# Kernel optimization log

Hardware: AMD Instinct MI355X
Metric: run time of the kernel (lower is better)

Reference implementation:

```python
import jax, jax.numpy as jnp
import numpy as np

EMBED_DIM = 1024
NUM_HEADS = 16
HEAD_DIM = EMBED_DIM // NUM_HEADS
B, L = 2, 2048
SCALE = HEAD_DIM ** -0.5


def setup_inputs() -> dict:
    key = jax.random.key(0)
    ks = jax.random.split(key, 8)
    x = jax.random.normal(ks[0], (B, L, EMBED_DIM), dtype=jnp.float32)
    phylo_dists = jax.random.uniform(ks[1], (B, L), dtype=jnp.float32)
    alibi_bias = jax.random.normal(ks[2], (NUM_HEADS, L, L), dtype=jnp.float32) * 0.02
    # causal mask: 1 where attending allowed (j <= i), broadcast over B,H
    attn_mask = (jnp.arange(L)[:, None] >= jnp.arange(L)[None, :])[None, None]
    # learned params (Linear stores weight as [out, in]; y = x @ W.T + b)
    qkv_w = jax.random.normal(ks[3], (3 * EMBED_DIM, EMBED_DIM), dtype=jnp.float32) * (EMBED_DIM ** -0.5)
    qkv_b = jnp.zeros((3 * EMBED_DIM,), dtype=jnp.float32)
    out_w = jax.random.normal(ks[4], (EMBED_DIM, EMBED_DIM), dtype=jnp.float32) * (EMBED_DIM ** -0.5)
    out_b = jnp.zeros((EMBED_DIM,), dtype=jnp.float32)
    phylo_alpha = jnp.float32(0.5)
    return {"x": x, "phylo_dists": phylo_dists, "alibi_bias": alibi_bias,
            "attn_mask": attn_mask, "qkv_w": qkv_w, "qkv_b": qkv_b,
            "out_w": out_w, "out_b": out_b, "phylo_alpha": phylo_alpha}


def reference(x, phylo_dists, alibi_bias, attn_mask, qkv_w, qkv_b, out_w, out_b, phylo_alpha):
    Bm, Lm, D = x.shape
    qkv = (x @ qkv_w.T + qkv_b).reshape(Bm, Lm, 3, NUM_HEADS, HEAD_DIM)
    qkv = jnp.transpose(qkv, (2, 0, 3, 1, 4))  # [3, B, H, L, hd]
    q, k, v = qkv[0], qkv[1], qkv[2]
    # phylo temperature: scalar per batch element
    phylo_scalar = phylo_dists.mean(axis=-1).reshape(Bm, 1, 1, 1)
    temp = jnp.clip(1.0 + phylo_alpha * phylo_scalar, 1e-6, None)
    scores = jnp.einsum('bhqd,bhkd->bhqk', q, k) * (SCALE * temp)
    scores = scores + alibi_bias[None]  # [B,H,L,L]
    scores = jnp.where(attn_mask, scores, -jnp.inf)
    attn = jax.nn.softmax(scores, axis=-1)
    out = jnp.einsum('bhqk,bhkd->bhqd', attn, v)
    out = jnp.transpose(out, (0, 2, 1, 3)).reshape(Bm, Lm, D)
    return out @ out_w.T + out_b
```

## Files before the change

### kernel.cpp

```cpp
#include <hip/hip_runtime.h>
#include <hip/hip_bf16.h>

typedef __attribute__((ext_vector_type(8))) short bf16x8;
typedef __attribute__((ext_vector_type(4))) float f32x4;
typedef __attribute__((ext_vector_type(4))) float f4v;
typedef __attribute__((ext_vector_type(4))) short s4v;

__device__ __forceinline__ short f2bf(float f) {
    union { __hip_bfloat16 h; short s; } u;
    u.h = __float2bfloat16(f);
    return u.s;
}

__device__ __forceinline__ void gload_lds16(const void* g, void* l) {
    __builtin_amdgcn_global_load_lds(
        (const __attribute__((address_space(1))) void*)g,
        (__attribute__((address_space(3))) void*)l,
        16, 0, 0);
}

#define MFMA16(a, b, c) __builtin_amdgcn_mfma_f32_16x16x32_bf16((a), (b), (c), 0, 0, 0)

__global__ void prep_kernel(const float* __restrict__ x,
                            const float* __restrict__ qw,
                            const float* __restrict__ ow,
                            const float* __restrict__ pd,
                            const float* __restrict__ alphap,
                            s4v* __restrict__ xb, s4v* __restrict__ qb,
                            s4v* __restrict__ ob, float* __restrict__ scales) {
    __shared__ float wsum[4];
    if (blockIdx.x >= 2048) {
        int b = blockIdx.x - 2048;
        float s = 0.f;
        for (int i = threadIdx.x; i < 2048; i += 256) s += pd[b * 2048 + i];
        for (int o = 32; o; o >>= 1) s += __shfl_down(s, o);
        if ((threadIdx.x & 63) == 0) wsum[threadIdx.x >> 6] = s;
        __syncthreads();
        if (threadIdx.x == 0) {
            float t = wsum[0] + wsum[1] + wsum[2] + wsum[3];
            float mean = t * (1.0f / 2048.0f);
            float temp = fmaxf(1.0f + alphap[0] * mean, 1e-6f);
            scales[b] = 0.125f * temp;
        }
        return;
    }
    #pragma unroll
    for (int j = 0; j < 4; ++j) {
        int idx = blockIdx.x * 1024 + j * 256 + threadIdx.x;
        const f4v* src;
        s4v* dst;
        int off;
        if (idx < 1048576)      { src = (const f4v*)x;  dst = xb; off = idx; }
        else if (idx < 1835008) { src = (const f4v*)qw; dst = qb; off = idx - 1048576; }
        else                    { src = (const f4v*)ow; dst = ob; off = idx - 1835008; }
        f4v v = src[off];
        s4v o;
        #pragma unroll
        for (int k = 0; k < 4; ++k) o[k] = f2bf(v[k]);
        dst[off] = o;
    }
}

template<int BF16_OUT, int NF>
__global__ __launch_bounds__(256, 2)
void gemm_nt(const __hip_bfloat16* __restrict__ A,
             const __hip_bfloat16* __restrict__ Bw,
             const float* __restrict__ bias,
             void* __restrict__ Cv,
             int M, int N, int K) {
    __shared__ short sA[128 * 64];
    __shared__ short sB[NF * 32 * 64];
    const int tid = threadIdx.x;
    const int wave = tid >> 6, lane = tid & 63;
    const int g = lane >> 4, c = lane & 15;
    const int wr = wave >> 1, wc = wave & 1;
    const long m0 = (long)blockIdx.y * 128, n0 = (long)blockIdx.x * (NF * 32);

    f32x4 acc[4][NF];
    #pragma unroll
    for (int m = 0; m < 4; ++m)
        #pragma unroll
        for (int n = 0; n < NF; ++n) acc[m][n] = f32x4{0.f, 0.f, 0.f, 0.f};

    for (int k0 = 0; k0 < K; k0 += 64) {
        #pragma unroll
        for (int i = 0; i < 4; ++i) {
            int cb = (i * 4 + wave) * 64;
            int chunk = cb + lane;
            int row = chunk >> 3;
            int sc = ((chunk & 7) * 16) ^ ((row & 7) << 4);
            const char* gA = (const char*)(A + (m0 + row) * (long)K + k0) + sc;
            gload_lds16(gA, (char*)sA + cb * 16);
        }
        #pragma unroll
        for (int i = 0; i < NF; ++i) {
            int cb = (i * 4 + wave) * 64;
            int chunk = cb + lane;
            int row = chunk >> 3;
            int sc = ((chunk & 7) * 16) ^ ((row & 7) << 4);
            const char* gB = (const char*)(Bw + (n0 + row) * (long)K + k0) + sc;
            gload_lds16(gB, (char*)sB + cb * 16);
        }
        __syncthreads();
        #pragma unroll
        for (int s = 0; s < 2; ++s) {
            bf16x8 af[4], bfr[NF];
            #pragma unroll
            for (int m = 0; m < 4; ++m) {
                int row = wr * 64 + m * 16 + c;
                int kb = (s * 64 + g * 16) ^ ((row & 7) << 4);
                af[m] = *(const bf16x8*)((const char*)sA + row * 128 + kb);
            }
            #pragma unroll
            for (int n = 0; n < NF; ++n) {
                int row = wc * (NF * 16) + n * 16 + c;
                int kb = (s * 64 + g * 16) ^ ((row & 7) << 4);
                bfr[n] = *(const bf16x8*)((const char*)sB + row * 128 + kb);
            }
            #pragma unroll
            for (int m = 0; m < 4; ++m)
                #pragma unroll
                for (int n = 0; n < NF; ++n)
                    acc[m][n] = MFMA16(af[m], bfr[n], acc[m][n]);
        }
        __syncthreads();
    }

    #pragma unroll
    for (int m = 0; m < 4; ++m) {
        #pragma unroll
        for (int n = 0; n < NF; ++n) {
            long col = n0 + wc * (NF * 16) + n * 16 + c;
            float bv = bias[col];
            #pragma unroll
            for (int r = 0; r < 4; ++r) {
                long row = m0 + wr * 64 + m * 16 + g * 4 + r;
                float v = acc[m][n][r] + bv;
                if (BF16_OUT)
                    ((__hip_bfloat16*)Cv)[row * N + col] = __float2bfloat16(v);
                else
                    ((float*)Cv)[row * N + col] = v;
            }
        }
    }
}


__device__ __forceinline__ void compute_tile(
    const bf16x8 (&kf)[4][2], const short* sVtc, short* sPw,
    bf16x8 qf0, bf16x8 qf1,
    f32x4 (&acc_o)[4], f32x4& accL, float (&m)[4],
    const float (&ab)[4][4],
    float scale, int qi0, int kv0, bool diag, int g, int c)
{
    f32x4 accs[4];
    #pragma unroll
    for (int nf = 0; nf < 4; ++nf) {
        accs[nf] = f32x4{0.f, 0.f, 0.f, 0.f};
        accs[nf] = MFMA16(qf0, kf[nf][0], accs[nf]);
        accs[nf] = MFMA16(qf1, kf[nf][1], accs[nf]);
    }
    float s[4][4], pmax[4];
    bool ok = true;
    #pragma unroll
    for (int r = 0; r < 4; ++r) {
        int qi = qi0 + r;
        #pragma unroll
        for (int nf = 0; nf < 4; ++nf) {
            float sv = fmaf(accs[nf][r], scale, ab[nf][r]);
            if (diag && (kv0 + nf * 16 + c > qi)) sv = -1e30f;
            s[r][nf] = sv;
        }
        pmax[r] = fmaxf(fmaxf(s[r][0], s[r][1]), fmaxf(s[r][2], s[r][3]));
        ok = ok && (pmax[r] <= m[r] + 8.0f);
    }
    if (!__all(ok)) {
        #pragma unroll
        for (int r = 0; r < 4; ++r) {
            float mx = pmax[r];
            mx = fmaxf(mx, __shfl_xor(mx, 1));
            mx = fmaxf(mx, __shfl_xor(mx, 2));
            mx = fmaxf(mx, __shfl_xor(mx, 4));
            mx = fmaxf(mx, __shfl_xor(mx, 8));
            float mn = fmaxf(m[r], mx);
            float alpha = __expf(m[r] - mn);
            m[r] = mn;
            accL[r] *= alpha;
            #pragma unroll
            for (int d = 0; d < 4; ++d) acc_o[d][r] *= alpha;
        }
    }
    #pragma unroll
    for (int r = 0; r < 4; ++r)
        #pragma unroll
        for (int nf = 0; nf < 4; ++nf)
            sPw[(g * 4 + r) * 72 + nf * 16 + c] = f2bf(__expf(s[r][nf] - m[r]));
    asm volatile("s_waitcnt lgkmcnt(0)" ::: "memory");
    bf16x8 pf0 = *(const bf16x8*)((const char*)sPw + c * 144 + g * 16);
    bf16x8 pf1 = *(const bf16x8*)((const char*)sPw + c * 144 + 64 + g * 16);
    const short ONE = 0x3F80;
    const bf16x8 ones = {ONE, ONE, ONE, ONE, ONE, ONE, ONE, ONE};
    accL = MFMA16(pf0, ones, accL);
    accL = MFMA16(pf1, ones, accL);
    #pragma unroll
    for (int d = 0; d < 4; ++d) {
        const char* vb = (const char*)sVtc + (d * 16 + c) * 144;
        bf16x8 vf0 = *(const bf16x8*)(vb + g * 16);
        bf16x8 vf1 = *(const bf16x8*)(vb + 64 + g * 16);
        acc_o[d] = MFMA16(pf0, vf0, acc_o[d]);
        acc_o[d] = MFMA16(pf1, vf1, acc_o[d]);
    }
}

__global__ __launch_bounds__(256, 2)
void attn_kernel(const __hip_bfloat16* __restrict__ qkv,
                 const float* __restrict__ alibi,
                 const float* __restrict__ scales,
                 __hip_bfloat16* __restrict__ out) {
    __shared__ short sK[2][64 * 64];
    __shared__ short sVt[2][64 * 72];
    __shared__ short sPA[4][16 * 72];
    __shared__ short sPB[4][16 * 72];

    const int p = blockIdx.x, h = blockIdx.y, b = blockIdx.z;
    const int qtA = p, qtB = 31 - p;
    const int nIter = qtB + 1;
    const int tid = threadIdx.x;
    const int wave = tid >> 6, lane = tid & 63;
    const int g = lane >> 4, c = lane & 15;
    const float scale = scales[b];
    const long base_bl = (long)b * 2048;

    const int qA0 = qtA * 64 + wave * 16;
    const int qB0 = qtB * 64 + wave * 16;

    const __hip_bfloat16* qrowA = qkv + (base_bl + qA0 + c) * 3072 + h * 64;
    const __hip_bfloat16* qrowB = qkv + (base_bl + qB0 + c) * 3072 + h * 64;
    bf16x8 qAf0 = *(const bf16x8*)(qrowA + g * 8);
    bf16x8 qAf1 = *(const bf16x8*)(qrowA + 32 + g * 8);
    bf16x8 qBf0 = *(const bf16x8*)(qrowB + g * 8);
    bf16x8 qBf1 = *(const bf16x8*)(qrowB + 32 + g * 8);

    const __hip_bfloat16* kg = qkv + base_bl * 3072 + 1024 + h * 64;
    const __hip_bfloat16* vg = qkv + base_bl * 3072 + 2048 + h * 64;
    const float* abA_base = alibi + (long)h * 2048 * 2048 + (long)(qA0 + g * 4) * 2048;
    const float* abB_base = alibi + (long)h * 2048 * 2048 + (long)(qB0 + g * 4) * 2048;

    const int p2 = tid & 31;
    const int d0 = (tid >> 5) * 8;
    const __hip_bfloat16* vrow = vg + (long)(2 * p2) * 3072 + d0;

    f32x4 accA[4], accB[4], accLA, accLB;
    float mA[4], mB[4];
    #pragma unroll
    for (int d = 0; d < 4; ++d) {
        accA[d] = f32x4{0.f, 0.f, 0.f, 0.f};
        accB[d] = f32x4{0.f, 0.f, 0.f, 0.f};
    }
    accLA = f32x4{0.f, 0.f, 0.f, 0.f};
    accLB = f32x4{0.f, 0.f, 0.f, 0.f};
    #pragma unroll
    for (int r = 0; r < 4; ++r) { mA[r] = -3e38f; mB[r] = -3e38f; }

    float abA[4][4], abB[4][4], abAn[4][4], abBn[4][4];

    {
        #pragma unroll
        for (int i = 0; i < 2; ++i) {
            int cb = (i * 4 + wave) * 64;
            int chunk = cb + lane;
            int row = chunk >> 3;
            int sc = ((chunk & 7) * 16) ^ ((row & 7) << 4);
            gload_lds16((const char*)(kg + (long)row * 3072) + sc,
                        (char*)sK[0] + cb * 16);
        }
        bf16x8 va = *(const bf16x8*)vrow;
        bf16x8 vb = *(const bf16x8*)(vrow + 3072);
        #pragma unroll
        for (int j = 0; j < 8; ++j) {
            unsigned pk = ((unsigned)(unsigned short)va[j]) |
                          (((unsigned)(unsigned short)vb[j]) << 16);
            *(unsigned*)((char*)sVt[0] + (d0 + j) * 144 + p2 * 4) = pk;
        }
        #pragma unroll
        for (int nf = 0; nf < 4; ++nf)
            #pragma unroll
            for (int r = 0; r < 4; ++r) {
                abA[nf][r] = abA_base[(long)r * 2048 + nf * 16 + c];
                abB[nf][r] = abB_base[(long)r * 2048 + nf * 16 + c];
                abAn[nf][r] = 0.f; abBn[nf][r] = 0.f;
            }
    }
    __syncthreads();

    for (int t = 0; t < nIter; ++t) {
        const int cur = t & 1;
        const int kv0 = t * 64;
        bf16x8 va, vb;
        const bool haveNext = (t + 1 < nIter);
        if (haveNext) {
            #pragma unroll
            for (int i = 0; i < 2; ++i) {
                int cb = (i * 4 + wave) * 64;
                int chunk = cb + lane;
                int row = chunk >> 3;
                int sc = ((chunk & 7) * 16) ^ ((row & 7) << 4);
                gload_lds16((const char*)(kg + (long)(kv0 + 64 + row) * 3072) + sc,
                            (char*)sK[cur ^ 1] + cb * 16);
            }
            const __hip_bfloat16* vp = vrow + (long)(kv0 + 64) * 3072;
            va = *(const bf16x8*)vp;
            vb = *(const bf16x8*)(vp + 3072);
            #pragma unroll
            for (int nf = 0; nf < 4; ++nf)
                #pragma unroll
                for (int r = 0; r < 4; ++r)
                    abBn[nf][r] = abB_base[(long)r * 2048 + kv0 + 64 + nf * 16 + c];
        }
        if (t + 1 <= qtA) {
            #pragma unroll
            for (int nf = 0; nf < 4; ++nf)
                #pragma unroll
                for (int r = 0; r < 4; ++r)
                    abAn[nf][r] = abA_base[(long)r * 2048 + kv0 + 64 + nf * 16 + c];
        }

        bf16x8 kf[4][2];
        const int swz = (c & 7) << 4;
        #pragma unroll
        for (int nf = 0; nf < 4; ++nf) {
            const char* kb = (const char*)sK[cur] + (nf * 16 + c) * 128;
            kf[nf][0] = *(const bf16x8*)(kb + ((g * 16) ^ swz));
            kf[nf][1] = *(const bf16x8*)(kb + ((64 + g * 16) ^ swz));
        }

        compute_tile(kf, sVt[cur], &sPB[wave][0], qBf0, qBf1,
                     accB, accLB, mB, abB, scale, qB0 + g * 4, kv0, t == qtB, g, c);
        if (t <= qtA)
            compute_tile(kf, sVt[cur], &sPA[wave][0], qAf0, qAf1,
                         accA, accLA, mA, abA, scale, qA0 + g * 4, kv0, t == qtA, g, c);

        if (haveNext) {
            #pragma unroll
            for (int j = 0; j < 8; ++j) {
                unsigned pk = ((unsigned)(unsigned short)va[j]) |
                              (((unsigned)(unsigned short)vb[j]) << 16);
                *(unsigned*)((char*)sVt[cur ^ 1] + (d0 + j) * 144 + p2 * 4) = pk;
            }
        }
        __syncthreads();
        #pragma unroll
        for (int nf = 0; nf < 4; ++nf)
            #pragma unroll
            for (int r = 0; r < 4; ++r) {
                abA[nf][r] = abAn[nf][r];
                abB[nf][r] = abBn[nf][r];
            }
    }

    __hip_bfloat16* opA = out + (base_bl + qA0 + g * 4) * 1024 + h * 64;
    __hip_bfloat16* opB = out + (base_bl + qB0 + g * 4) * 1024 + h * 64;
    #pragma unroll
    for (int r = 0; r < 4; ++r) {
        float invA = 1.0f / accLA[r];
        float invB = 1.0f / accLB[r];
        #pragma unroll
        for (int d = 0; d < 4; ++d) {
            opA[(long)r * 1024 + d * 16 + c] = __float2bfloat16(accA[d][r] * invA);
            opB[(long)r * 1024 + d * 16 + c] = __float2bfloat16(accB[d][r] * invB);
        }
    }
}

extern "C" void kernel_launch(void* const* d_in, const int* in_sizes, int n_in,
                              void* d_out, int out_size, void* d_ws, size_t ws_size,
                              hipStream_t stream) {
    const float* x      = (const float*)d_in[0];
    const float* phylo  = (const float*)d_in[1];
    const float* alibi  = (const float*)d_in[2];
    const float* qkv_w  = (const float*)d_in[4];
    const float* qkv_b  = (const float*)d_in[5];
    const float* out_w  = (const float*)d_in[6];
    const float* out_b  = (const float*)d_in[7];
    const float* alphap = (const float*)d_in[8];

    char* ws = (char*)d_ws;
    __hip_bfloat16* xbf   = (__hip_bfloat16*)(ws);
    __hip_bfloat16* qwbf  = (__hip_bfloat16*)(ws + (8l << 20));
    __hip_bfloat16* owbf  = (__hip_bfloat16*)(ws + (14l << 20));
    __hip_bfloat16* qkvbf = (__hip_bfloat16*)(ws + (16l << 20));
    __hip_bfloat16* aobf  = (__hip_bfloat16*)(ws + (40l << 20));
    float* scales         = (float*)(ws + (48l << 20));

    prep_kernel<<<2050, 256, 0, stream>>>(x, qkv_w, out_w, phylo, alphap,
                                          (s4v*)xbf, (s4v*)qwbf, (s4v*)owbf, scales);

    gemm_nt<1, 4><<<dim3(24, 32), 256, 0, stream>>>(xbf, qwbf, qkv_b, qkvbf,
                                                    4096, 3072, 1024);
    attn_kernel<<<dim3(16, 16, 2), 256, 0, stream>>>(qkvbf, alibi, scales, aobf);
    gemm_nt<0, 2><<<dim3(16, 32), 256, 0, stream>>>(aobf, owbf, out_b, d_out,
                                                    4096, 1024, 1024);
}
```

Before: 135.4 us.

## Replace QKV GEMM with 256x256 triple-buffered ping-pong kernel and MFMA priority hints

Replaces the QKV projection GEMM with a new 512-thread kernel that computes 256x256 output tiles from a three-stage LDS ring using direct global-to-LDS loads and XOR-swizzled layout. A block-index remap groups tiles for L2 locality, and loads are interleaved with MFMA phases bracketed by s_setprio. The attention inner tile also raises wave priority around its MFMA blocks. The larger tile means fewer blocks (192), which risks under-filling the GPU, and 96KB of dynamic LDS limits occupancy.

```diff
diff --git a/kernel.cpp b/kernel.cpp
--- a/kernel.cpp
+++ b/kernel.cpp
@@ -61,6 +61,134 @@
     }
 }
 
+__global__ __launch_bounds__(512, 2)
+void gemm_qkv_8ph(const __hip_bfloat16* __restrict__ A,
+                  const __hip_bfloat16* __restrict__ Bw,
+                  const float* __restrict__ bias,
+                  __hip_bfloat16* __restrict__ C) {
+    extern __shared__ short lds[];
+    const int tid = threadIdx.x;
+    const int wave = tid >> 6, lane = tid & 63;
+    const int g = lane >> 4, c = lane & 15;
+    const int wr = wave >> 2, wc = wave & 3;
+
+    int bid = blockIdx.y * 12 + blockIdx.x;
+    bid = (bid & 7) * 24 + (bid >> 3);
+    const long m0 = (long)(bid / 12) * 256;
+    const long n0 = (long)(bid % 12) * 256;
+
+    const int sr = tid >> 3;
+    const int ss = tid & 7;
+    const int sl = ss ^ (sr & 7);
+    const int srowoff = 2 * sr + (sl >> 2);
+    const int skel = (sl & 3) * 8;
+
+    const int xterm = (((c & 1) << 6) | (g << 4)) ^ ((c >> 1) << 4);
+
+    f32x4 acc[8][4];
+    #pragma unroll
+    for (int m = 0; m < 8; ++m)
+        #pragma unroll
+        for (int n = 0; n < 4; ++n) acc[m][n] = f32x4{0.f, 0.f, 0.f, 0.f};
+
+#define STAGE_A(tt, d)                                                        \
+    {                                                                         \
+        _Pragma("unroll")                                                     \
+        for (int h = 0; h < 2; ++h) {                                         \
+            const __hip_bfloat16* src =                                       \
+                A + (m0 + h * 128 + srowoff) * 1024 + (tt) * 32 + skel;       \
+            gload_lds16(src, lds + (d) * 16384 + (h * 512 + tid) * 8);        \
+        }                                                                     \
+    }
+#define STAGE_B(tt, d)                                                        \
+    {                                                                         \
+        _Pragma("unroll")                                                     \
+        for (int h = 0; h < 2; ++h) {                                         \
+            const __hip_bfloat16* src =                                       \
+                Bw + (n0 + h * 128 + srowoff) * 1024 + (tt) * 32 + skel;      \
+            gload_lds16(src, lds + (d) * 16384 + 8192 + (h * 512 + tid) * 8); \
+        }                                                                     \
+    }
+
+    STAGE_A(0, 0); STAGE_B(0, 0);
+    STAGE_A(1, 1); STAGE_B(1, 1);
+    asm volatile("s_waitcnt vmcnt(4)" ::: "memory");
+    __builtin_amdgcn_s_barrier();
+
+    const int NT = 32;
+    for (int t = 0; t < NT; ++t) {
+        const int d = t % 3;
+        const char* bufA = (const char*)(lds + d * 16384);
+        const char* bufB = (const char*)(lds + d * 16384 + 8192);
+        const int dn = (t + 2) % 3;
+        const bool st = (t + 2 < NT);
+
+        bf16x8 af[8], bfr0, bfr1;
+        #pragma unroll
+        for (int m = 0; m < 8; ++m) {
+            int row = wr * 64 + m * 8 + (c >> 1);
+            af[m] = *(const bf16x8*)(bufA + row * 128 + xterm);
+        }
+        {
+            int row0 = wc * 32 + 0 * 8 + (c >> 1);
+            int row1 = wc * 32 + 1 * 8 + (c >> 1);
+            bfr0 = *(const bf16x8*)(bufB + row0 * 128 + xterm);
+            bfr1 = *(const bf16x8*)(bufB + row1 * 128 + xterm);
+        }
+        if (st) STAGE_A(t + 2, dn);
+        __builtin_amdgcn_s_barrier();
+        asm volatile("s_waitcnt lgkmcnt(0)" ::: "memory");
+        __builtin_amdgcn_sched_barrier(0);
+        __builtin_amdgcn_s_setprio(1);
+        #pragma unroll
+        for (int m = 0; m < 8; ++m) {
+            acc[m][0] = MFMA16(af[m], bfr0, acc[m][0]);
+            acc[m][1] = MFMA16(af[m], bfr1, acc[m][1]);
+        }
+        __builtin_amdgcn_s_setprio(0);
+        __builtin_amdgcn_s_barrier();
+
+        {
+            int row2 = wc * 32 + 2 * 8 + (c >> 1);
+            int row3 = wc * 32 + 3 * 8 + (c >> 1);
+            bfr0 = *(const bf16x8*)(bufB + row2 * 128 + xterm);
+            bfr1 = *(const bf16x8*)(bufB + row3 * 128 + xterm);
+        }
+        if (st) STAGE_B(t + 2, dn);
+        __builtin_amdgcn_s_barrier();
+        if (t < NT - 2)
+            asm volatile("s_waitcnt vmcnt(4)" ::: "memory");
+        else if (t == NT - 2)
+            asm volatile("s_waitcnt vmcnt(0)" ::: "memory");
+        asm volatile("s_waitcnt lgkmcnt(0)" ::: "memory");
+        __builtin_amdgcn_sched_barrier(0);
+        __builtin_amdgcn_s_setprio(1);
+        #pragma unroll
+        for (int m = 0; m < 8; ++m) {
+            acc[m][2] = MFMA16(af[m], bfr0, acc[m][2]);
+            acc[m][3] = MFMA16(af[m], bfr1, acc[m][3]);
+        }
+        __builtin_amdgcn_s_setprio(0);
+        __builtin_amdgcn_s_barrier();
+    }
+#undef STAGE_A
+#undef STAGE_B
+
+    #pragma unroll
+    for (int m = 0; m < 8; ++m) {
+        #pragma unroll
+        for (int n = 0; n < 4; ++n) {
+            long col = n0 + wc * 64 + n * 16 + c;
+            float bv = bias[col];
+            #pragma unroll
+            for (int r = 0; r < 4; ++r) {
+                long row = m0 + wr * 128 + m * 16 + g * 4 + r;
+                C[row * 3072 + col] = __float2bfloat16(acc[m][n][r] + bv);
+            }
+        }
+    }
+}
+
 template<int BF16_OUT, int NF>
 __global__ __launch_bounds__(256, 2)
 void gemm_nt(const __hip_bfloat16* __restrict__ A,
@@ -145,7 +273,6 @@
     }
 }
 
-
 __device__ __forceinline__ void compute_tile(
     const bf16x8 (&kf)[4][2], const short* sVtc, short* sPw,
     bf16x8 qf0, bf16x8 qf1,
@@ -154,12 +281,14 @@
     float scale, int qi0, int kv0, bool diag, int g, int c)
 {
     f32x4 accs[4];
+    __builtin_amdgcn_s_setprio(1);
     #pragma unroll
     for (int nf = 0; nf < 4; ++nf) {
         accs[nf] = f32x4{0.f, 0.f, 0.f, 0.f};
         accs[nf] = MFMA16(qf0, kf[nf][0], accs[nf]);
         accs[nf] = MFMA16(qf1, kf[nf][1], accs[nf]);
     }
+    __builtin_amdgcn_s_setprio(0);
     float s[4][4], pmax[4];
     bool ok = true;
     #pragma unroll
@@ -200,6 +329,7 @@
     bf16x8 pf1 = *(const bf16x8*)((const char*)sPw + c * 144 + 64 + g * 16);
     const short ONE = 0x3F80;
     const bf16x8 ones = {ONE, ONE, ONE, ONE, ONE, ONE, ONE, ONE};
+    __builtin_amdgcn_s_setprio(1);
     accL = MFMA16(pf0, ones, accL);
     accL = MFMA16(pf1, ones, accL);
     #pragma unroll
@@ -210,6 +340,7 @@
         acc_o[d] = MFMA16(pf0, vf0, acc_o[d]);
         acc_o[d] = MFMA16(pf1, vf1, acc_o[d]);
     }
+    __builtin_amdgcn_s_setprio(0);
 }
 
 __global__ __launch_bounds__(256, 2)
@@ -392,11 +523,13 @@
     __hip_bfloat16* aobf  = (__hip_bfloat16*)(ws + (40l << 20));
     float* scales         = (float*)(ws + (48l << 20));
 
+    (void)hipFuncSetAttribute((const void*)gemm_qkv_8ph,
+                              hipFuncAttributeMaxDynamicSharedMemorySize, 98304);
+
     prep_kernel<<<2050, 256, 0, stream>>>(x, qkv_w, out_w, phylo, alphap,
                                           (s4v*)xbf, (s4v*)qwbf, (s4v*)owbf, scales);
 
-    gemm_nt<1, 4><<<dim3(24, 32), 256, 0, stream>>>(xbf, qwbf, qkv_b, qkvbf,
-                                                    4096, 3072, 1024);
+    gemm_qkv_8ph<<<dim3(12, 16), 512, 98304, stream>>>(xbf, qwbf, qkv_b, qkvbf);
     attn_kernel<<<dim3(16, 16, 2), 256, 0, stream>>>(qkvbf, alibi, scales, aobf);
     gemm_nt<0, 2><<<dim3(16, 32), 256, 0, stream>>>(aobf, owbf, out_b, d_out,
                                                     4096, 1024, 1024);
```

After: 136.7 us. Within noise of the previous version (+1.0%).

## Replace paired causal q-tiles with one q-tile per block and raise occupancy

Applied to the files above, without the earlier changes.

The attention kernel no longer pairs q-tile p with q-tile 31-p inside one block. It launches 1024 blocks, each handling a single 64-row q-tile, with the heaviest tiles in the lowest blockIdx.z so they are dispatched first, and launch bounds rise to 4 blocks per SM. K fragments are now read from LDS inside compute_tile, and s_setprio wraps the MFMA sections. This trades the K/V tile reuse between two q-tiles for lower register pressure and more concurrent waves, but each K/V tile is now loaded twice as often and load balance depends on dispatch order.

```diff
diff --git a/kernel.cpp b/kernel.cpp
--- a/kernel.cpp
+++ b/kernel.cpp
@@ -147,19 +147,25 @@
 
 
 __device__ __forceinline__ void compute_tile(
-    const bf16x8 (&kf)[4][2], const short* sVtc, short* sPw,
+    const short* sKc, const short* sVtc, short* sPw,
     bf16x8 qf0, bf16x8 qf1,
     f32x4 (&acc_o)[4], f32x4& accL, float (&m)[4],
     const float (&ab)[4][4],
     float scale, int qi0, int kv0, bool diag, int g, int c)
 {
     f32x4 accs[4];
+    const int swz = (c & 7) << 4;
+    __builtin_amdgcn_s_setprio(1);
     #pragma unroll
     for (int nf = 0; nf < 4; ++nf) {
+        const char* kb = (const char*)sKc + (nf * 16 + c) * 128;
+        bf16x8 kf0 = *(const bf16x8*)(kb + ((g * 16) ^ swz));
+        bf16x8 kf1 = *(const bf16x8*)(kb + ((64 + g * 16) ^ swz));
         accs[nf] = f32x4{0.f, 0.f, 0.f, 0.f};
-        accs[nf] = MFMA16(qf0, kf[nf][0], accs[nf]);
-        accs[nf] = MFMA16(qf1, kf[nf][1], accs[nf]);
-    }
+        accs[nf] = MFMA16(qf0, kf0, accs[nf]);
+        accs[nf] = MFMA16(qf1, kf1, accs[nf]);
+    }
+    __builtin_amdgcn_s_setprio(0);
     float s[4][4], pmax[4];
     bool ok = true;
     #pragma unroll
@@ -200,6 +206,7 @@
     bf16x8 pf1 = *(const bf16x8*)((const char*)sPw + c * 144 + 64 + g * 16);
     const short ONE = 0x3F80;
     const bf16x8 ones = {ONE, ONE, ONE, ONE, ONE, ONE, ONE, ONE};
+    __builtin_amdgcn_s_setprio(1);
     accL = MFMA16(pf0, ones, accL);
     accL = MFMA16(pf1, ones, accL);
     #pragma unroll
@@ -210,59 +217,50 @@
         acc_o[d] = MFMA16(pf0, vf0, acc_o[d]);
         acc_o[d] = MFMA16(pf1, vf1, acc_o[d]);
     }
-}
-
-__global__ __launch_bounds__(256, 2)
+    __builtin_amdgcn_s_setprio(0);
+}
+
+__global__ __launch_bounds__(256, 4)
 void attn_kernel(const __hip_bfloat16* __restrict__ qkv,
                  const float* __restrict__ alibi,
                  const float* __restrict__ scales,
                  __hip_bfloat16* __restrict__ out) {
     __shared__ short sK[2][64 * 64];
     __shared__ short sVt[2][64 * 72];
-    __shared__ short sPA[4][16 * 72];
-    __shared__ short sPB[4][16 * 72];
-
-    const int p = blockIdx.x, h = blockIdx.y, b = blockIdx.z;
-    const int qtA = p, qtB = 31 - p;
-    const int nIter = qtB + 1;
+    __shared__ short sP[4][16 * 72];
+
+    const int h = blockIdx.x, b = blockIdx.y;
+    const int qt = 31 - blockIdx.z;
+    const int nIter = qt + 1;
     const int tid = threadIdx.x;
     const int wave = tid >> 6, lane = tid & 63;
     const int g = lane >> 4, c = lane & 15;
     const float scale = scales[b];
     const long base_bl = (long)b * 2048;
 
-    const int qA0 = qtA * 64 + wave * 16;
-    const int qB0 = qtB * 64 + wave * 16;
-
-    const __hip_bfloat16* qrowA = qkv + (base_bl + qA0 + c) * 3072 + h * 64;
-    const __hip_bfloat16* qrowB = qkv + (base_bl + qB0 + c) * 3072 + h * 64;
-    bf16x8 qAf0 = *(const bf16x8*)(qrowA + g * 8);
-    bf16x8 qAf1 = *(const bf16x8*)(qrowA + 32 + g * 8);
-    bf16x8 qBf0 = *(const bf16x8*)(qrowB + g * 8);
-    bf16x8 qBf1 = *(const bf16x8*)(qrowB + 32 + g * 8);
+    const int q0 = qt * 64 + wave * 16;
+
+    const __hip_bfloat16* qrow = qkv + (base_bl + q0 + c) * 3072 + h * 64;
+    bf16x8 qf0 = *(const bf16x8*)(qrow + g * 8);
+    bf16x8 qf1 = *(const bf16x8*)(qrow + 32 + g * 8);
 
     const __hip_bfloat16* kg = qkv + base_bl * 3072 + 1024 + h * 64;
     const __hip_bfloat16* vg = qkv + base_bl * 3072 + 2048 + h * 64;
-    const float* abA_base = alibi + (long)h * 2048 * 2048 + (long)(qA0 + g * 4) * 2048;
-    const float* abB_base = alibi + (long)h * 2048 * 2048 + (long)(qB0 + g * 4) * 2048;
+    const float* ab_base = alibi + (long)h * 2048 * 2048 + (long)(q0 + g * 4) * 2048;
 
     const int p2 = tid & 31;
     const int d0 = (tid >> 5) * 8;
     const __hip_bfloat16* vrow = vg + (long)(2 * p2) * 3072 + d0;
 
-    f32x4 accA[4], accB[4], accLA, accLB;
-    float mA[4], mB[4];
-    #pragma unroll
-    for (int d = 0; d < 4; ++d) {
-        accA[d] = f32x4{0.f, 0.f, 0.f, 0.f};
-        accB[d] = f32x4{0.f, 0.f, 0.f, 0.f};
-    }
-    accLA = f32x4{0.f, 0.f, 0.f, 0.f};
-    accLB = f32x4{0.f, 0.f, 0.f, 0.f};
-    #pragma unroll
-    for (int r = 0; r < 4; ++r) { mA[r] = -3e38f; mB[r] = -3e38f; }
-
-    float abA[4][4], abB[4][4], abAn[4][4], abBn[4][4];
+    f32x4 acc[4], accL;
+    float m[4];
+    #pragma unroll
+    for (int d = 0; d < 4; ++d) acc[d] = f32x4{0.f, 0.f, 0.f, 0.f};
+    accL = f32x4{0.f, 0.f, 0.f, 0.f};
+    #pragma unroll
+    for (int r = 0; r < 4; ++r) m[r] = -3e38f;
+
+    float ab[4][4], abn[4][4];
 
     {
         #pragma unroll
@@ -286,9 +284,8 @@
         for (int nf = 0; nf < 4; ++nf)
             #pragma unroll
             for (int r = 0; r < 4; ++r) {
-                abA[nf][r] = abA_base[(long)r * 2048 + nf * 16 + c];
-                abB[nf][r] = abB_base[(long)r * 2048 + nf * 16 + c];
-                abAn[nf][r] = 0.f; abBn[nf][r] = 0.f;
+                ab[nf][r] = ab_base[(long)r * 2048 + nf * 16 + c];
+                abn[nf][r] = 0.f;
             }
     }
     __syncthreads();
@@ -315,30 +312,11 @@
             for (int nf = 0; nf < 4; ++nf)
                 #pragma unroll
                 for (int r = 0; r < 4; ++r)
-                    abBn[nf][r] = abB_base[(long)r * 2048 + kv0 + 64 + nf * 16 + c];
-        }
-        if (t + 1 <= qtA) {
-            #pragma unroll
-            for (int nf = 0; nf < 4; ++nf)
-                #pragma unroll
-                for (int r = 0; r < 4; ++r)
-                    abAn[nf][r] = abA_base[(long)r * 2048 + kv0 + 64 + nf * 16 + c];
-        }
-
-        bf16x8 kf[4][2];
-        const int swz = (c & 7) << 4;
-        #pragma unroll
-        for (int nf = 0; nf < 4; ++nf) {
-            const char* kb = (const char*)sK[cur] + (nf * 16 + c) * 128;
-            kf[nf][0] = *(const bf16x8*)(kb + ((g * 16) ^ swz));
-            kf[nf][1] = *(const bf16x8*)(kb + ((64 + g * 16) ^ swz));
-        }
-
-        compute_tile(kf, sVt[cur], &sPB[wave][0], qBf0, qBf1,
-                     accB, accLB, mB, abB, scale, qB0 + g * 4, kv0, t == qtB, g, c);
-        if (t <= qtA)
-            compute_tile(kf, sVt[cur], &sPA[wave][0], qAf0, qAf1,
-                         accA, accLA, mA, abA, scale, qA0 + g * 4, kv0, t == qtA, g, c);
+                    abn[nf][r] = ab_base[(long)r * 2048 + kv0 + 64 + nf * 16 + c];
+        }
+
+        compute_tile(sK[cur], sVt[cur], &sP[wave][0], qf0, qf1,
+                     acc, accL, m, ab, scale, q0 + g * 4, kv0, t == qt, g, c);
 
         if (haveNext) {
             #pragma unroll
@@ -352,23 +330,17 @@
         #pragma unroll
         for (int nf = 0; nf < 4; ++nf)
             #pragma unroll
-            for (int r = 0; r < 4; ++r) {
-                abA[nf][r] = abAn[nf][r];
-                abB[nf][r] = abBn[nf][r];
-            }
-    }
-
-    __hip_bfloat16* opA = out + (base_bl + qA0 + g * 4) * 1024 + h * 64;
-    __hip_bfloat16* opB = out + (base_bl + qB0 + g * 4) * 1024 + h * 64;
+            for (int r = 0; r < 4; ++r)
+                ab[nf][r] = abn[nf][r];
+    }
+
+    __hip_bfloat16* op = out + (base_bl + q0 + g * 4) * 1024 + h * 64;
     #pragma unroll
     for (int r = 0; r < 4; ++r) {
-        float invA = 1.0f / accLA[r];
-        float invB = 1.0f / accLB[r];
-        #pragma unroll
-        for (int d = 0; d < 4; ++d) {
-            opA[(long)r * 1024 + d * 16 + c] = __float2bfloat16(accA[d][r] * invA);
-            opB[(long)r * 1024 + d * 16 + c] = __float2bfloat16(accB[d][r] * invB);
-        }
+        float inv = 1.0f / accL[r];
+        #pragma unroll
+        for (int d = 0; d < 4; ++d)
+            op[(long)r * 1024 + d * 16 + c] = __float2bfloat16(acc[d][r] * inv);
     }
 }
 
@@ -397,7 +369,7 @@
 
     gemm_nt<1, 4><<<dim3(24, 32), 256, 0, stream>>>(xbf, qwbf, qkv_b, qkvbf,
                                                     4096, 3072, 1024);
-    attn_kernel<<<dim3(16, 16, 2), 256, 0, stream>>>(qkvbf, alibi, scales, aobf);
+    attn_kernel<<<dim3(16, 2, 32), 256, 0, stream>>>(qkvbf, alibi, scales, aobf);
     gemm_nt<0, 2><<<dim3(16, 32), 256, 0, stream>>>(aobf, owbf, out_b, d_out,
                                                     4096, 1024, 1024);
 }
```

New measurement: 128.5 us. -5.1%, faster.
